# Kernel optimization log

Hardware: AMD Instinct MI355X
Metric: run time of the kernel (lower is better)

The kernel has to match this reference:

```python
import jax, jax.numpy as jnp
import numpy as np
import math

BASE_RES, MAX_RES, NUM_LOD, FEAT_DIM = 16, 256, 8, 2
_growth = math.exp((math.log(MAX_RES) - math.log(BASE_RES)) / (NUM_LOD - 1))
LODS = [int(BASE_RES * _growth ** L) for L in range(NUM_LOD)]
N_PTS = 4_000_000


def setup_inputs() -> dict:
    key = jax.random.key(0)
    keys = jax.random.split(key, NUM_LOD + 1)
    inp = {"pts": jax.random.uniform(keys[0], (N_PTS, 2), dtype=jnp.float32)}
    for i, res in enumerate(LODS):
        inp[f"cb{i}"] = jax.random.normal(keys[i + 1], (res * res, FEAT_DIM), dtype=jnp.float32) * 0.01
    return inp


def _forward(pts, codebooks):
    feats = []
    for res, cb in zip(LODS, codebooks):
        # 'closest' interpolation: floor to nearest lower grid cell, row-major index
        xy = jnp.floor(pts * (res - 1)).astype(jnp.int32)  # [N, 2]
        idx = xy[:, 0] + xy[:, 1] * res                    # [N]
        feats.append(cb[idx])                              # [N, feat_dim]
    # torch: cat of unsqueeze(-1) -> [N, feat_dim, num_lod], then reshape
    all_features = jnp.stack(feats, axis=-1)               # [N, feat_dim, num_lod]
    return all_features.reshape(-1, NUM_LOD * FEAT_DIM)


def reference(pts, cb0, cb1, cb2, cb3, cb4, cb5, cb6, cb7):
    return _forward(pts, (cb0, cb1, cb2, cb3, cb4, cb5, cb6, cb7))
```

## Files before the change

### kernel.cpp

```cpp
#include <hip/hip_runtime.h>
#include <math.h>

#define NUM_LOD 8
#define NLDS 3
#define BLOCK 512
#define PPT 2
#define TPAD 17

struct GridParams {
    const float* cb[NUM_LOD];
    int res[NUM_LOD];
    int ldsOff[NLDS];
    int ldsCnt[NLDS];
};

__global__ __launch_bounds__(BLOCK) void densegrid_kernel(
    const float2* __restrict__ pts, GridParams p, float4* __restrict__ out4, long long n)
{
    __shared__ float cbLds[4096];
    __shared__ float tbuf[BLOCK * TPAD];

    const int t = threadIdx.x;

    for (int L = 0; L < NLDS; ++L) {
        const float2* src = (const float2*)p.cb[L];
        float2* dst = (float2*)&cbLds[p.ldsOff[L]];
        const int cnt2 = p.ldsCnt[L] >> 1;
        for (int j = t; j < cnt2; j += BLOCK) dst[j] = src[j];
    }
    __syncthreads();

    const long long base = (long long)blockIdx.x * (BLOCK * PPT);
    long long pi[PPT];
    float2 pt[PPT];
#pragma unroll
    for (int s = 0; s < PPT; ++s) {
        pi[s] = base + (long long)s * BLOCK + t;
        if (pi[s] < n) pt[s] = pts[pi[s]];
    }

    float o[PPT][16];
#pragma unroll
    for (int s = 0; s < PPT; ++s) {
        if (pi[s] >= n) continue;
#pragma unroll
        for (int L = 0; L < NUM_LOD; ++L) {
            const int   res = p.res[L];
            const float sc  = (float)(res - 1);
            const int ix = (int)floorf(pt[s].x * sc);
            const int iy = (int)floorf(pt[s].y * sc);
            const int idx = ix + iy * res;
            float2 f;
            if (L < NLDS) f = ((const float2*)&cbLds[p.ldsOff[L]])[idx];
            else          f = ((const float2*)p.cb[L])[idx];
            o[s][L]     = f.x;
            o[s][8 + L] = f.y;
        }
    }

    const long long lim4 = n * 4;
#pragma unroll
    for (int s = 0; s < PPT; ++s) {
        if (s > 0) __syncthreads();
        if (pi[s] < n) {
#pragma unroll
            for (int j = 0; j < 16; ++j) tbuf[t * TPAD + j] = o[s][j];
        }
        __syncthreads();
        const long long b4 = (base + (long long)s * BLOCK) * 4;
#pragma unroll
        for (int k = 0; k < 4; ++k) {
            const int m = k * BLOCK + t;
            const long long g = b4 + m;
            if (g < lim4) {
                const int pnt = m >> 2, q = m & 3;
                const float* src = &tbuf[pnt * TPAD + q * 4];
                out4[g] = make_float4(src[0], src[1], src[2], src[3]);
            }
        }
    }
}

extern "C" void kernel_launch(void* const* d_in, const int* in_sizes, int n_in,
                              void* d_out, int out_size, void* d_ws, size_t ws_size,
                              hipStream_t stream)
{
    const float2* pts = (const float2*)d_in[0];
    const long long n = in_sizes[0] / 2;

    GridParams p;
    int off = 0;
    for (int L = 0; L < NUM_LOD; ++L) {
        p.cb[L] = (const float*)d_in[L + 1];
        const int cells = in_sizes[L + 1] / 2;
        p.res[L] = (int)(sqrt((double)cells) + 0.5);
        if (L < NLDS) {
            p.ldsOff[L] = off;
            p.ldsCnt[L] = in_sizes[L + 1];
            off += in_sizes[L + 1];
        }
    }

    const long long grid = (n + (long long)(BLOCK * PPT) - 1) / (BLOCK * PPT);
    densegrid_kernel<<<(int)grid, BLOCK, 0, stream>>>(pts, p, (float4*)d_out, n);
}
```

Before: 342.7 us.

## Split LODs across thread pairs, drop LDS transpose, cache four LODs in LDS

Each point is now handled by two adjacent threads: even threads look up LODs 0-3 from shared memory and odd threads look up LODs 4-7 from global memory. Each thread writes two float4 directly, so the shared-memory transpose buffer and its barriers are gone. Blocks loop over several point groups to amortize the codebook preload, and the fourth LOD is now cached in LDS. The LDS and global paths sit on divergent branches within a wavefront, which serializes them.

```diff
diff --git a/kernel.cpp b/kernel.cpp
--- a/kernel.cpp
+++ b/kernel.cpp
@@ -2,10 +2,10 @@
 #include <math.h>
 
 #define NUM_LOD 8
-#define NLDS 3
+#define NLDS 4
 #define BLOCK 512
-#define PPT 2
-#define TPAD 17
+#define ITERS 4
+#define LDS_F 9428
 
 struct GridParams {
     const float* cb[NUM_LOD];
@@ -14,12 +14,10 @@
     int ldsCnt[NLDS];
 };
 
-__global__ __launch_bounds__(BLOCK) void densegrid_kernel(
+__global__ __launch_bounds__(BLOCK, 8) void densegrid_kernel(
     const float2* __restrict__ pts, GridParams p, float4* __restrict__ out4, long long n)
 {
-    __shared__ float cbLds[4096];
-    __shared__ float tbuf[BLOCK * TPAD];
-
+    __shared__ float cbLds[LDS_F];
     const int t = threadIdx.x;
 
     for (int L = 0; L < NLDS; ++L) {
@@ -30,53 +28,51 @@
     }
     __syncthreads();
 
-    const long long base = (long long)blockIdx.x * (BLOCK * PPT);
-    long long pi[PPT];
-    float2 pt[PPT];
+    const int half  = t & 1;
+    const int pslot = t >> 1;
+
+    float sc[4];
+    int   rs[4];
+    const float2* gptr[4];
+    int   loff[4];
 #pragma unroll
-    for (int s = 0; s < PPT; ++s) {
-        pi[s] = base + (long long)s * BLOCK + t;
-        if (pi[s] < n) pt[s] = pts[pi[s]];
+    for (int j = 0; j < 4; ++j) {
+        const int L = half ? (4 + j) : j;
+        rs[j]  = p.res[L];
+        sc[j]  = (float)(rs[j] - 1);
+        gptr[j] = (const float2*)p.cb[4 + j];
+        loff[j] = p.ldsOff[j] >> 1;
     }
 
-    float o[PPT][16];
+    const long long base = (long long)blockIdx.x * (BLOCK / 2) * ITERS;
+
+#pragma unroll 1
+    for (int it = 0; it < ITERS; ++it) {
+        const long long P = base + (long long)it * (BLOCK / 2) + pslot;
+        if (P < n) {
+            const float2 pt = pts[P];
+            float vx[4], vy[4];
+            if (half) {
 #pragma unroll
-    for (int s = 0; s < PPT; ++s) {
-        if (pi[s] >= n) continue;
+                for (int j = 0; j < 4; ++j) {
+                    const int ix = (int)(pt.x * sc[j]);
+                    const int iy = (int)(pt.y * sc[j]);
+                    const float2 f = gptr[j][ix + iy * rs[j]];
+                    vx[j] = f.x; vy[j] = f.y;
+                }
+            } else {
+                const float2* ldsF2 = (const float2*)cbLds;
 #pragma unroll
-        for (int L = 0; L < NUM_LOD; ++L) {
-            const int   res = p.res[L];
-            const float sc  = (float)(res - 1);
-            const int ix = (int)floorf(pt[s].x * sc);
-            const int iy = (int)floorf(pt[s].y * sc);
-            const int idx = ix + iy * res;
-            float2 f;
-            if (L < NLDS) f = ((const float2*)&cbLds[p.ldsOff[L]])[idx];
-            else          f = ((const float2*)p.cb[L])[idx];
-            o[s][L]     = f.x;
-            o[s][8 + L] = f.y;
-        }
-    }
-
-    const long long lim4 = n * 4;
-#pragma unroll
-    for (int s = 0; s < PPT; ++s) {
-        if (s > 0) __syncthreads();
-        if (pi[s] < n) {
-#pragma unroll
-            for (int j = 0; j < 16; ++j) tbuf[t * TPAD + j] = o[s][j];
-        }
-        __syncthreads();
-        const long long b4 = (base + (long long)s * BLOCK) * 4;
-#pragma unroll
-        for (int k = 0; k < 4; ++k) {
-            const int m = k * BLOCK + t;
-            const long long g = b4 + m;
-            if (g < lim4) {
-                const int pnt = m >> 2, q = m & 3;
-                const float* src = &tbuf[pnt * TPAD + q * 4];
-                out4[g] = make_float4(src[0], src[1], src[2], src[3]);
+                for (int j = 0; j < 4; ++j) {
+                    const int ix = (int)(pt.x * sc[j]);
+                    const int iy = (int)(pt.y * sc[j]);
+                    const float2 f = ldsF2[loff[j] + ix + iy * rs[j]];
+                    vx[j] = f.x; vy[j] = f.y;
+                }
             }
+            const long long m4 = (P << 2) + half;
+            out4[m4]     = make_float4(vx[0], vx[1], vx[2], vx[3]);
+            out4[m4 + 2] = make_float4(vy[0], vy[1], vy[2], vy[3]);
         }
     }
 }
@@ -101,6 +97,7 @@
         }
     }
 
-    const long long grid = (n + (long long)(BLOCK * PPT) - 1) / (BLOCK * PPT);
+    const long long ppb  = (long long)(BLOCK / 2) * ITERS;
+    const long long grid = (n + ppb - 1) / ppb;
     densegrid_kernel<<<(int)grid, BLOCK, 0, stream>>>(pts, p, (float4*)d_out, n);
 }
```

Result: slower. 384.2 us (+12.1%).
